# Optimization experiments

Measured on AMD Instinct MI355X. Metric: run time of the kernel, lower is better.

## Reference

```python
import jax, jax.numpy as jnp
import numpy as np

L = 10
DIL = tuple(2 ** i for i in range(L))  # dilations 1..512, kernel_size=2 -> one past tap, mem_size = dilation
DMAX = max(DIL)
R = 64            # residual channels
G = 2 * R         # gate channels (tanh | sigmoid)
S = 256           # skip channels
MEL = 80
NCLS = 256
HOP = 64
END = 256
FRAMES = 8


def setup_inputs() -> dict:
    ks = jax.random.split(jax.random.key(0), 16)
    sc = jnp.float32(0.1)
    n = lambda k, shape: jax.random.normal(k, shape, jnp.float32) * sc
    return {
        "y": jax.random.normal(ks[0], (MEL, FRAMES), jnp.float32),
        "samples": jax.random.uniform(ks[1], (FRAMES * HOP,), jnp.float32),
        "c": 1,
        "emb": jnp.tanh(n(ks[2], (NCLS, R))),               # buffer already tanh'ed in __init__
        "condition_W": n(ks[3], (L * G, MEL)),
        "WV_past_weight": n(ks[4], (L, G, R, 1)),            # kernel_size=2 -> 1 past tap
        "WV_present_weight": n(ks[5], (L, G, R)),
        "W_o_weight": n(ks[6], (L - 1, R + S, R)),
        "W_o_bias": n(ks[7], (L - 1, R + S)),
        "W_o_weight_last": n(ks[8], (S, R)),
        "W_o_bias_last": n(ks[9], (S,)),
        "end1_w": n(ks[10], (END, S)),
        "end1_b": n(ks[11], (END,)),
        "end2_w": n(ks[12], (NCLS, END)),
        "end2_b": n(ks[13], (NCLS,)),
    }


def _forward(y, samples, c, emb, condition_W, WV_past, WV_pres, W_o_w, W_o_b,
             W_o_wl, W_o_bl, e1w, e1b, e2w, e2b):
    # nearest-neighbor upsample of conditioning by hop_length (F.interpolate default mode)
    y_up = jnp.repeat(y, HOP, axis=1)                        # [MEL, T]
    T = y_up.shape[1]
    conds = (condition_W @ y_up).T.reshape(T, L, G)          # precompute all conditioning projections
    dil = jnp.array(DIL, jnp.int32)
    lidx = jnp.arange(L)

    def step(carry, xs):
        hist, prev = carry                                   # hist: [L, R, DMAX] shared ring buffer, global write ptr t%DMAX
        t, cond_t, s = xs
        x = emb[prev]                                        # [R]
        # value written dil[j] steps ago (zeros before warm-up), read before this step's write
        past = hist[lidx, :, (t - dil) % DMAX]               # [L, R]
        skip = jnp.zeros((S,), hist.dtype)
        written = []
        for j in range(L):
            h = cond_t[j] + WV_past[j, :, :, 0] @ past[j] + WV_pres[j] @ x
            zw, zf = jnp.split(h, 2)
            z = jnp.tanh(zw) * jax.nn.sigmoid(zf)
            written.append(x)                                # layer j stores its input in its ring buffer
            if j < L - 1:
                o = W_o_w[j] @ z + W_o_b[j]
                x = x + o[:R]
                skip = skip + o[R:]
            else:
                skip = skip + W_o_wl @ z + W_o_bl
        hist = hist.at[:, :, t % DMAX].set(jnp.stack(written))
        hid = jax.nn.relu(e1w @ jax.nn.relu(skip) + e1b)
        logits = (e2w @ hid + e2b) * c
        # inverse-CDF sampling: first index where cumsum(softmax) exceeds the uniform sample
        new = jnp.argmax(jnp.cumsum(jax.nn.softmax(logits)) > s).astype(jnp.int32)
        return (hist, new), (new, logits)

    carry0 = (jnp.zeros((L, R, DMAX), jnp.float32), jnp.int32(NCLS // 2 - 1))
    _, (outs, logits) = jax.lax.scan(step, carry0, (jnp.arange(T), conds, samples))
    return outs, logits


def reference(y, samples, c, emb, condition_W, WV_past_weight, WV_present_weight,
              W_o_weight, W_o_bias, W_o_weight_last, W_o_bias_last,
              end1_w, end1_b, end2_w, end2_b):
    outs, _ = _forward(y, samples, c, emb, condition_W, WV_past_weight,
                       WV_present_weight, W_o_weight, W_o_bias,
                       W_o_weight_last, W_o_bias_last, end1_w, end1_b, end2_w, end2_b)
    return outs
```

## Files before the change

### kernel.cpp

```cpp
#include <hip/hip_runtime.h>
#include <cmath>

#define L_     10
#define R_     64
#define G_     128
#define S_     256
#define MEL_   80
#define NCLS_  256
#define HOP_   64
#define END_   256
#define FRAMES_ 8
#define T_     512

typedef unsigned long long u64;

#define COND8_OFF   0
#define HIST_OFF    10240
#define MBX64_OFF   (HIST_OFF + 8*T_*R_)
#define CTR64_OFF   (MBX64_OFF + 4*R_*2)
#define HID64_OFF   (CTR64_OFF + 10*S_*2)
#define FLAG_OFF    (HID64_OFF + S_*2)

#define FID_PREV   11
#define FID_CLAIM  12

#define NROLE 7
#define SPIN_CAP (1 << 16)

__device__ __forceinline__ void push_tag(u64* p, float v, int tag) {
  u64 pk = ((u64)(unsigned)tag << 32) | (unsigned)__float_as_int(v);
  asm volatile("global_atomic_swap_x2 %0, %1, off" :: "v"(p), "v"(pk) : "memory");
}
__device__ __forceinline__ float poll_tag(u64* p, int want) {
  u64 r; int n = 0;
  do {
    asm volatile("global_atomic_add_x2 %0, %1, %2, off sc0\n\ts_waitcnt vmcnt(0)"
                 : "=&v"(r) : "v"(p), "v"(0ULL) : "memory");
    if ((int)(r >> 32) >= want) break;
  } while (++n <= SPIN_CAP);
  return __int_as_float((int)(unsigned)(r & 0xffffffffULL));
}
__device__ __forceinline__ float2 poll_tag2(u64* p0, u64* p1, int want) {
  u64 r0, r1; int n = 0;
  for (;;) {
    asm volatile("global_atomic_add_x2 %0, %2, %4, off sc0\n\t"
                 "global_atomic_add_x2 %1, %3, %4, off sc0\n\t"
                 "s_waitcnt vmcnt(0)"
                 : "=&v"(r0), "=&v"(r1) : "v"(p0), "v"(p1), "v"(0ULL) : "memory");
    if ((int)(r0 >> 32) >= want && (int)(r1 >> 32) >= want) break;
    if (++n > SPIN_CAP) break;
  }
  return make_float2(__int_as_float((int)(unsigned)(r0 & 0xffffffffULL)),
                     __int_as_float((int)(unsigned)(r1 & 0xffffffffULL)));
}
__device__ __forceinline__ int flag_poll_atomic(int* p) {
  int v;
  asm volatile("global_atomic_add %0, %1, %2, off sc0\n\ts_waitcnt vmcnt(0)"
               : "=&v"(v) : "v"(p), "v"(0) : "memory");
  return v;
}
__device__ __forceinline__ void push_flag(int* p, int v) {
  asm volatile("global_atomic_swap %0, %1, off" :: "v"(p), "v"(v) : "memory");
}
__device__ __forceinline__ int wait_prev_wave(int* p, int want, int lane) {
  int v = 0, n = 0;
  do {
    if (lane == 0) v = flag_poll_atomic(p);
    v = __shfl(v, 0, 64);
    if ((v >> 16) >= want) break;
  } while (++n <= SPIN_CAP);
  return v & 0xffff;
}

#define DOTREG(N4, W, V4, ACC) do { \
  _Pragma("unroll") \
  for (int k_ = 0; k_ < (N4); ++k_) { float4 a_ = (V4)[k_]; \
    ACC = fmaf((W)[4*k_+0], a_.x, ACC); ACC = fmaf((W)[4*k_+1], a_.y, ACC); \
    ACC = fmaf((W)[4*k_+2], a_.z, ACC); ACC = fmaf((W)[4*k_+3], a_.w, ACC); } \
} while (0)

#define DOTREG_RELU(N4, W, V4, ACC) do { \
  _Pragma("unroll") \
  for (int k_ = 0; k_ < (N4); ++k_) { float4 a_ = (V4)[k_]; \
    a_.x = fmaxf(a_.x, 0.f); a_.y = fmaxf(a_.y, 0.f); \
    a_.z = fmaxf(a_.z, 0.f); a_.w = fmaxf(a_.w, 0.f); \
    ACC = fmaf((W)[4*k_+0], a_.x, ACC); ACC = fmaf((W)[4*k_+1], a_.y, ACC); \
    ACC = fmaf((W)[4*k_+2], a_.z, ACC); ACC = fmaf((W)[4*k_+3], a_.w, ACC); } \
} while (0)

__global__ void cond_prep_kernel(const float* __restrict__ condW,
                                 const float* __restrict__ y,
                                 float* __restrict__ cond8) {
  int idx = blockIdx.x * blockDim.x + threadIdx.x;
  if (idx >= FRAMES_ * L_ * G_) return;
  int f = idx / (L_ * G_);
  int row = idx - f * (L_ * G_);
  float acc = 0.f;
  for (int m = 0; m < MEL_; ++m)
    acc = fmaf(condW[row * MEL_ + m], y[m * FRAMES_ + f], acc);
  cond8[f * (L_ * G_) + row] = acc;
}

__global__ __launch_bounds__(256, 1) void wavenet_pipe(
    const float* __restrict__ samples,
    const int*   __restrict__ c_ptr,
    const float* __restrict__ emb,
    const float* __restrict__ WVp,
    const float* __restrict__ WVx,
    const float* __restrict__ Wo,
    const float* __restrict__ Wob,
    const float* __restrict__ Wol,
    const float* __restrict__ Wobl,
    const float* __restrict__ e1w,
    const float* __restrict__ e1b,
    const float* __restrict__ e2w,
    const float* __restrict__ e2b,
    float* __restrict__ ws,
    int*   __restrict__ out) {

  const int tid = threadIdx.x;

  float* cond8   = ws + COND8_OFF;
  float* hist    = ws + HIST_OFF;
  u64*   mbx     = (u64*)(ws + MBX64_OFF);
  u64*   contrib = (u64*)(ws + CTR64_OFF);
  u64*   mbhid   = (u64*)(ws + HID64_OFF);
  int*   flags   = (int*)(ws + FLAG_OFF);
  int*   fprev   = flags + FID_PREV * 16;

  __shared__ __align__(16) float x_s[R_];
  __shared__ __align__(16) float xb_s[R_];
  __shared__ __align__(16) float z_s[R_];
  __shared__ __align__(16) float zb_s[R_];
  __shared__ __align__(16) float cond_a_s[FRAMES_ * G_];
  __shared__ __align__(16) float cond_b_s[FRAMES_ * G_];
  __shared__ __align__(16) float biasC_s[10 * S_];
  __shared__ __align__(16) float vec_s[S_];
  __shared__ float wred[4], wsum[4];
  __shared__ int wcand[4];
  __shared__ int role_s;

  {
    unsigned xcc;
    asm volatile("s_getreg_b32 %0, hwreg(HW_REG_XCC_ID)" : "=s"(xcc));
    if (tid == 0) {
      int r = -1;
      if (xcc == 0) {
        int c0 = atomicAdd(flags + FID_CLAIM * 16, 1);
        if (c0 < NROLE) r = c0;
      }
      role_s = r;
    }
    __syncthreads();
  }
  const int bid = role_s;
  if (bid < 0) return;

  if (bid < 5) {
    const int k = bid;
    const int j_a = 2 * k, j_b = 2 * k + 1;
    const int dil_a = 1 << j_a, dil_b = 1 << j_b;
    const int gr = tid >> 1, gh = tid & 1;

    float wxa_w[32], wxa_f[32], wxb_w[32], wxb_f[32];
    float woa0[64], wob0[64], wex[64];
    float ba0, bb0;
    if (tid < 128) {
      const float4* p;
      p = (const float4*)(WVx + ((size_t)(j_a * G_ + gr)) * R_ + gh * 32);
      #pragma unroll
      for (int i = 0; i < 8; ++i) ((float4*)wxa_w)[i] = p[i];
      p = (const float4*)(WVx + ((size_t)(j_a * G_ + gr + 64)) * R_ + gh * 32);
      #pragma unroll
      for (int i = 0; i < 8; ++i) ((float4*)wxa_f)[i] = p[i];
      p = (const float4*)(WVx + ((size_t)(j_b * G_ + gr)) * R_ + gh * 32);
      #pragma unroll
      for (int i = 0; i < 8; ++i) ((float4*)wxb_w)[i] = p[i];
      p = (const float4*)(WVx + ((size_t)(j_b * G_ + gr + 64)) * R_ + gh * 32);
      #pragma unroll
      for (int i = 0; i < 8; ++i) ((float4*)wxb_f)[i] = p[i];
    }
    {
      const float* q = Wo + ((size_t)(j_a * (R_ + S_) + tid)) * R_;
      #pragma unroll
      for (int i = 0; i < 64; ++i) woa0[i] = q[i];
      ba0 = Wob[j_a * (R_ + S_) + tid];
      if (k < 4) {
        q = Wo + ((size_t)(j_b * (R_ + S_) + tid)) * R_;
        #pragma unroll
        for (int i = 0; i < 64; ++i) wob0[i] = q[i];
        bb0 = Wob[j_b * (R_ + S_) + tid];
      } else {
        q = Wol + (size_t)tid * R_;
        #pragma unroll
        for (int i = 0; i < 64; ++i) wob0[i] = q[i];
        bb0 = 0.f;
      }
      if (tid < 64) {
        q = Wo + ((size_t)(j_a * (R_ + S_) + 256 + tid)) * R_;
        #pragma unroll
        for (int i = 0; i < 64; ++i) wex[i] = q[i];
      } else if (tid < 128 && k < 4) {
        q = Wo + ((size_t)(j_b * (R_ + S_) + 256 + (tid - 64))) * R_;
        #pragma unroll
        for (int i = 0; i < 64; ++i) wex[i] = q[i];
      }
    }
    for (int i = tid; i < FRAMES_ * G_; i += 256) {
      cond_a_s[i] = cond8[(i >> 7) * (L_ * G_) + j_a * G_ + (i & 127)];
      cond_b_s[i] = cond8[(i >> 7) * (L_ * G_) + j_b * G_ + (i & 127)];
    }
    __syncthreads();
    float pd_aw = 0.f, pd_af = 0.f, pd_bw = 0.f, pd_bf = 0.f;
    if (tid < 128 && gh == 0) {
      pd_aw = cond_a_s[gr]; pd_af = cond_a_s[gr + 64];
      pd_bw = cond_b_s[gr]; pd_bf = cond_b_s[gr + 64];
    }

    float* hist_a = (k > 0) ? (hist + (size_t)(j_a - 1) * T_ * R_) : nullptr;
    float* hist_b = (k < 4) ? (hist + (size_t)(j_b - 1) * T_ * R_) : nullptr;
    u64* mbx_in    = mbx + (size_t)(k - 1) * R_;
    u64* mbx_out   = mbx + (size_t)k * R_;
    u64* contrib_a = contrib + (size_t)j_a * S_;
    u64* contrib_b = contrib + (size_t)j_b * S_;

    for (int t = 0; t < T_; ++t) {
      if (tid < 64) {
        if (k == 0) {
          int prev = 127;
          if (t > 0) prev = wait_prev_wave(fprev, t, tid);
          if (tid < 16)
            ((float4*)x_s)[tid] = ((const float4*)(emb + (size_t)prev * R_))[tid];
        } else {
          x_s[tid] = poll_tag(mbx_in + tid, t + 1);
        }
      }
      __syncthreads();

      if (tid < 128) {
        const float4* xs4 = (const float4*)(x_s + gh * 32);
        float vw = 0.f, vf = 0.f;
        DOTREG(8, wxa_w, xs4, vw);
        DOTREG(8, wxa_f, xs4, vf);
        vw += __shfl_down(vw, 1, 2);
        vf += __shfl_down(vf, 1, 2);
        if (gh == 0) {
          float hw = vw + pd_aw, hf = vf + pd_af;
          z_s[gr] = tanhf(hw) * (1.f / (1.f + expf(-hf)));
        }
      }
      if (hist_a && tid >= 240)
        ((float4*)(hist_a + (size_t)t * R_))[tid - 240] = ((const float4*)x_s)[tid - 240];
      __syncthreads();

      float va_keep = 0.f;
      {
        const float4* z4 = (const float4*)z_s;
        if (tid < 64) {
          float v0 = 0.f, v1 = 0.f;
          DOTREG(16, woa0, z4, v0);
          DOTREG(16, wex, z4, v1);
          xb_s[tid] = x_s[tid] + v0 + ba0;
          va_keep = v1;
        } else {
          float v0 = 0.f;
          DOTREG(16, woa0, z4, v0);
          va_keep = v0;
        }
      }
      __syncthreads();

      if (tid < 128) {
        const float4* xs4 = (const float4*)(xb_s + gh * 32);
        float vw = 0.f, vf = 0.f;
        DOTREG(8, wxb_w, xs4, vw);
        DOTREG(8, wxb_f, xs4, vf);
        vw += __shfl_down(vw, 1, 2);
        vf += __shfl_down(vf, 1, 2);
        if (gh == 0) {
          float hw = vw + pd_bw, hf = vf + pd_bf;
          zb_s[gr] = tanhf(hw) * (1.f / (1.f + expf(-hf)));
        }
      }
      if (hist_b && tid >= 240)
        ((float4*)(hist_b + (size_t)t * R_))[tid - 240] = ((const float4*)xb_s)[tid - 240];
      __syncthreads();

      {
        const float4* zb4 = (const float4*)zb_s;
        float v0 = 0.f;
        DOTREG(16, wob0, zb4, v0);
        if (k < 4) {
          if (tid < 64) {
            push_tag(mbx_out + tid, xb_s[tid] + v0 + bb0, t + 1);
            push_tag(contrib_a + 192 + tid, va_keep, t + 1);
          } else if (tid < 128) {
            float v1 = 0.f;
            DOTREG(16, wex, zb4, v1);
            push_tag(contrib_a + (tid - 64), va_keep, t + 1);
            push_tag(contrib_b + (tid - 64), v0, t + 1);
            push_tag(contrib_b + 192 + (tid - 64), v1, t + 1);
          } else {
            push_tag(contrib_a + (tid - 64), va_keep, t + 1);
            push_tag(contrib_b + (tid - 64), v0, t + 1);
          }
        } else {
          if (tid < 64) {
            push_tag(contrib_b + tid, v0, t + 1);
            push_tag(contrib_a + 192 + tid, va_keep, t + 1);
          } else {
            push_tag(contrib_a + (tid - 64), va_keep, t + 1);
            push_tag(contrib_b + tid, v0, t + 1);
          }
        }
      }

      const int tn = t + 1;
      if (tn < T_ && tid < 128) {
        const int f1 = tn >> 6;
        float wpw[32], wpf[32], pa[32];
        {
          const float4* pw = (const float4*)(WVp + ((size_t)(j_a * G_ + gr)) * R_ + gh * 32);
          const float4* pf = (const float4*)(WVp + ((size_t)(j_a * G_ + gr + 64)) * R_ + gh * 32);
          #pragma unroll
          for (int i = 0; i < 8; ++i) { ((float4*)wpw)[i] = pw[i]; ((float4*)wpf)[i] = pf[i]; }
          if (k == 0) {
            #pragma unroll
            for (int i = 0; i < 8; ++i) ((float4*)pa)[i] = ((const float4*)(x_s + gh * 32))[i];
          } else {
            const int tp = tn - dil_a;
            if (tp >= 0) {
              const float4* hp = (const float4*)(hist_a + (size_t)tp * R_ + gh * 32);
              #pragma unroll
              for (int i = 0; i < 8; ++i) ((float4*)pa)[i] = hp[i];
            } else {
              #pragma unroll
              for (int i = 0; i < 32; ++i) pa[i] = 0.f;
            }
          }
          float vw = 0.f, vf = 0.f;
          const float4* pa4 = (const float4*)pa;
          DOTREG(8, wpw, pa4, vw);
          DOTREG(8, wpf, pa4, vf);
          vw += __shfl_down(vw, 1, 2);
          vf += __shfl_down(vf, 1, 2);
          if (gh == 0) {
            pd_aw = vw + cond_a_s[f1 * G_ + gr];
            pd_af = vf + cond_a_s[f1 * G_ + gr + 64];
          }
        }
        if (k < 4) {
          const float4* pw = (const float4*)(WVp + ((size_t)(j_b * G_ + gr)) * R_ + gh * 32);
          const float4* pf = (const float4*)(WVp + ((size_t)(j_b * G_ + gr + 64)) * R_ + gh * 32);
          #pragma unroll
          for (int i = 0; i < 8; ++i) { ((float4*)wpw)[i] = pw[i]; ((float4*)wpf)[i] = pf[i]; }
          const int tp = tn - dil_b;
          if (tp >= 0) {
            const float4* hp = (const float4*)(hist_b + (size_t)tp * R_ + gh * 32);
            #pragma unroll
            for (int i = 0; i < 8; ++i) ((float4*)pa)[i] = hp[i];
          } else {
            #pragma unroll
            for (int i = 0; i < 32; ++i) pa[i] = 0.f;
          }
          float vw = 0.f, vf = 0.f;
          const float4* pa4 = (const float4*)pa;
          DOTREG(8, wpw, pa4, vw);
          DOTREG(8, wpf, pa4, vf);
          vw += __shfl_down(vw, 1, 2);
          vf += __shfl_down(vf, 1, 2);
          if (gh == 0) {
            pd_bw = vw + cond_b_s[f1 * G_ + gr];
            pd_bf = vf + cond_b_s[f1 * G_ + gr + 64];
          }
        } else {
          if (gh == 0) {
            pd_bw = cond_b_s[f1 * G_ + gr];
            pd_bf = cond_b_s[f1 * G_ + gr + 64];
          }
        }
      }
      __syncthreads();
    }

  } else if (bid == 5) {
    const int o_loc = tid >> 1, halfc = tid & 1;
    float w0[128], w1[128];
    {
      const float* p = e1w + ((size_t)o_loc) * S_ + halfc * 128;
      #pragma unroll
      for (int i = 0; i < 128; ++i) w0[i] = p[i];
      p = e1w + ((size_t)(128 + o_loc)) * S_ + halfc * 128;
      #pragma unroll
      for (int i = 0; i < 128; ++i) w1[i] = p[i];
    }
    const float bias0 = e1b[o_loc], bias1 = e1b[128 + o_loc];
    for (int i = tid; i < 10 * S_; i += 256) {
      int j = i >> 8, s = i & 255;
      biasC_s[i] = (j < 9) ? Wob[j * (R_ + S_) + 64 + s] : Wobl[s];
    }
    __syncthreads();

    for (int t = 0; t < T_; ++t) {
      float sacc = 0.f;
      for (int kk = 0; kk < 5; ++kk) {
        float2 v = poll_tag2(contrib + (size_t)(2 * kk) * S_ + tid,
                             contrib + (size_t)(2 * kk + 1) * S_ + tid, t + 1);
        sacc = (sacc + v.x) + biasC_s[(2 * kk) * S_ + tid];
        sacc = (sacc + v.y) + biasC_s[(2 * kk + 1) * S_ + tid];
      }
      vec_s[tid] = sacc;
      __syncthreads();
      const float4* s4 = (const float4*)(vec_s + halfc * 128);
      float v0 = 0.f, v1 = 0.f;
      DOTREG_RELU(32, w0, s4, v0);
      v0 += __shfl_down(v0, 1, 2);
      DOTREG_RELU(32, w1, s4, v1);
      v1 += __shfl_down(v1, 1, 2);
      if (halfc == 0) {
        push_tag(mbhid + o_loc,       fmaxf(v0 + bias0, 0.f), t + 1);
        push_tag(mbhid + 128 + o_loc, fmaxf(v1 + bias1, 0.f), t + 1);
      }
      __syncthreads();
    }

  } else {
    const int o_loc = tid >> 1, halfc = tid & 1;
    const float cf = (float)c_ptr[0];
    float w0[128], w1[128];
    {
      const float* p = e2w + ((size_t)o_loc) * END_ + halfc * 128;
      #pragma unroll
      for (int i = 0; i < 128; ++i) w0[i] = p[i];
      p = e2w + ((size_t)(128 + o_loc)) * END_ + halfc * 128;
      #pragma unroll
      for (int i = 0; i < 128; ++i) w1[i] = p[i];
    }
    const float bias0 = e2b[o_loc], bias1 = e2b[128 + o_loc];
    float* logits_s = cond_b_s;
    const int lane = tid & 63, wv = tid >> 6;

    for (int t = 0; t < T_; ++t) {
      vec_s[tid] = poll_tag(mbhid + tid, t + 1);
      __syncthreads();
      const float4* h4 = (const float4*)(vec_s + halfc * 128);
      float v0 = 0.f, v1 = 0.f;
      DOTREG(32, w0, h4, v0);
      v0 += __shfl_down(v0, 1, 2);
      DOTREG(32, w1, h4, v1);
      v1 += __shfl_down(v1, 1, 2);
      if (halfc == 0) {
        logits_s[o_loc]       = (v0 + bias0) * cf;
        logits_s[128 + o_loc] = (v1 + bias1) * cf;
      }
      __syncthreads();

      float lg = logits_s[tid];
      float m = lg;
      #pragma unroll
      for (int off = 32; off >= 1; off >>= 1) m = fmaxf(m, __shfl_xor(m, off, 64));
      if (lane == 0) wred[wv] = m;
      __syncthreads();
      m = fmaxf(fmaxf(wred[0], wred[1]), fmaxf(wred[2], wred[3]));
      float e = expf(lg - m);
      float cs = e;
      #pragma unroll
      for (int off = 1; off < 64; off <<= 1) {
        float o_ = __shfl_up(cs, off, 64);
        if (lane >= off) cs += o_;
      }
      if (lane == 63) wsum[wv] = cs;
      __syncthreads();
      float total = wsum[0] + wsum[1] + wsum[2] + wsum[3];
      float offv = 0.f;
      for (int w2 = 0; w2 < wv; ++w2) offv += wsum[w2];
      float thresh = samples[t] * total;
      bool flagb = (offv + cs) > thresh;
      unsigned long long mk = __ballot(flagb);
      if (lane == 0) wcand[wv] = mk ? (wv * 64 + __ffsll(mk) - 1) : 100000;
      __syncthreads();
      if (tid == 0) {
        int nw = min(min(wcand[0], wcand[1]), min(wcand[2], wcand[3]));
        if (nw >= 100000) nw = 0;
        out[t] = nw;
        push_flag(fprev, ((t + 1) << 16) | nw);
      }
      __syncthreads();
    }
  }
}

extern "C" void kernel_launch(void* const* d_in, const int* in_sizes, int n_in,
                              void* d_out, int out_size, void* d_ws, size_t ws_size,
                              hipStream_t stream) {
  const float* y       = (const float*)d_in[0];
  const float* samples = (const float*)d_in[1];
  const int*   c       = (const int*)d_in[2];
  const float* emb     = (const float*)d_in[3];
  const float* condW   = (const float*)d_in[4];
  const float* WVp     = (const float*)d_in[5];
  const float* WVx     = (const float*)d_in[6];
  const float* Wo      = (const float*)d_in[7];
  const float* Wob     = (const float*)d_in[8];
  const float* Wol     = (const float*)d_in[9];
  const float* Wobl    = (const float*)d_in[10];
  const float* e1w     = (const float*)d_in[11];
  const float* e1b     = (const float*)d_in[12];
  const float* e2w     = (const float*)d_in[13];
  const float* e2b     = (const float*)d_in[14];

  float* ws  = (float*)d_ws;
  int*   out = (int*)d_out;

  hipMemsetAsync((char*)d_ws + (size_t)FLAG_OFF * sizeof(float), 0,
                 16 * 16 * sizeof(int), stream);

  cond_prep_kernel<<<(FRAMES_ * L_ * G_ + 255) / 256, 256, 0, stream>>>(
      condW, y, ws + COND8_OFF);

  wavenet_pipe<<<256, 256, 0, stream>>>(samples, c, emb, WVp, WVx, Wo, Wob,
                                        Wol, Wobl, e1w, e1b, e2w, e2b, ws, out);
}
```

Baseline: 8.852 ms.

## Split layer blocks into critical-path wave and helper waves synced via LDS counters

Within each two-layer block, one 64-thread wave now runs the serial residual chain (gate dots, residual projections, mailbox push) with full 64-wide weight rows in registers. The other three waves compute the skip contributions, the history writes and the next step's past-tap projections. The two groups coordinate through LDS atomic counters instead of block-wide __syncthreads, so only the critical chain sits on the inter-block latency path. The cost is the spin-wait overhead on the counters and heavier register use per lane, since each thread now computes a full 64-length dot product with no lane-pair split.

```diff
diff --git a/kernel.cpp b/kernel.cpp
--- a/kernel.cpp
+++ b/kernel.cpp
@@ -26,6 +26,7 @@
 
 #define NROLE 7
 #define SPIN_CAP (1 << 16)
+#define LDS_SPIN_CAP (1 << 17)
 
 __device__ __forceinline__ void push_tag(u64* p, float v, int tag) {
   u64 pk = ((u64)(unsigned)tag << 32) | (unsigned)__float_as_int(v);
@@ -70,6 +71,19 @@
     if ((v >> 16) >= want) break;
   } while (++n <= SPIN_CAP);
   return v & 0xffff;
+}
+
+__device__ __forceinline__ void lds_spin_ge(int* p, int want) {
+  int n = 0;
+  while (__hip_atomic_load(p, __ATOMIC_ACQUIRE, __HIP_MEMORY_SCOPE_WORKGROUP) < want) {
+    if (++n > LDS_SPIN_CAP) break;
+  }
+}
+__device__ __forceinline__ void lds_store_rel(int* p, int v) {
+  __hip_atomic_store(p, v, __ATOMIC_RELEASE, __HIP_MEMORY_SCOPE_WORKGROUP);
+}
+__device__ __forceinline__ void lds_add_rel(int* p) {
+  (void)__hip_atomic_fetch_add(p, 1, __ATOMIC_RELEASE, __HIP_MEMORY_SCOPE_WORKGROUP);
 }
 
 #define DOTREG(N4, W, V4, ACC) do { \
@@ -130,8 +144,10 @@
 
   __shared__ __align__(16) float x_s[R_];
   __shared__ __align__(16) float xb_s[R_];
-  __shared__ __align__(16) float z_s[R_];
-  __shared__ __align__(16) float zb_s[R_];
+  __shared__ __align__(16) float z_sa[R_];
+  __shared__ __align__(16) float z_sb[R_];
+  __shared__ __align__(16) float pd_sa[G_];
+  __shared__ __align__(16) float pd_sb[G_];
   __shared__ __align__(16) float cond_a_s[FRAMES_ * G_];
   __shared__ __align__(16) float cond_b_s[FRAMES_ * G_];
   __shared__ __align__(16) float biasC_s[10 * S_];
@@ -139,6 +155,7 @@
   __shared__ float wred[4], wsum[4];
   __shared__ int wcand[4];
   __shared__ int role_s;
+  __shared__ int zctr, cdone;
 
   {
     unsigned xcc;
@@ -150,6 +167,7 @@
         if (c0 < NROLE) r = c0;
       }
       role_s = r;
+      zctr = 0; cdone = 0;
     }
     __syncthreads();
   }
@@ -160,62 +178,6 @@
     const int k = bid;
     const int j_a = 2 * k, j_b = 2 * k + 1;
     const int dil_a = 1 << j_a, dil_b = 1 << j_b;
-    const int gr = tid >> 1, gh = tid & 1;
-
-    float wxa_w[32], wxa_f[32], wxb_w[32], wxb_f[32];
-    float woa0[64], wob0[64], wex[64];
-    float ba0, bb0;
-    if (tid < 128) {
-      const float4* p;
-      p = (const float4*)(WVx + ((size_t)(j_a * G_ + gr)) * R_ + gh * 32);
-      #pragma unroll
-      for (int i = 0; i < 8; ++i) ((float4*)wxa_w)[i] = p[i];
-      p = (const float4*)(WVx + ((size_t)(j_a * G_ + gr + 64)) * R_ + gh * 32);
-      #pragma unroll
-      for (int i = 0; i < 8; ++i) ((float4*)wxa_f)[i] = p[i];
-      p = (const float4*)(WVx + ((size_t)(j_b * G_ + gr)) * R_ + gh * 32);
-      #pragma unroll
-      for (int i = 0; i < 8; ++i) ((float4*)wxb_w)[i] = p[i];
-      p = (const float4*)(WVx + ((size_t)(j_b * G_ + gr + 64)) * R_ + gh * 32);
-      #pragma unroll
-      for (int i = 0; i < 8; ++i) ((float4*)wxb_f)[i] = p[i];
-    }
-    {
-      const float* q = Wo + ((size_t)(j_a * (R_ + S_) + tid)) * R_;
-      #pragma unroll
-      for (int i = 0; i < 64; ++i) woa0[i] = q[i];
-      ba0 = Wob[j_a * (R_ + S_) + tid];
-      if (k < 4) {
-        q = Wo + ((size_t)(j_b * (R_ + S_) + tid)) * R_;
-        #pragma unroll
-        for (int i = 0; i < 64; ++i) wob0[i] = q[i];
-        bb0 = Wob[j_b * (R_ + S_) + tid];
-      } else {
-        q = Wol + (size_t)tid * R_;
-        #pragma unroll
-        for (int i = 0; i < 64; ++i) wob0[i] = q[i];
-        bb0 = 0.f;
-      }
-      if (tid < 64) {
-        q = Wo + ((size_t)(j_a * (R_ + S_) + 256 + tid)) * R_;
-        #pragma unroll
-        for (int i = 0; i < 64; ++i) wex[i] = q[i];
-      } else if (tid < 128 && k < 4) {
-        q = Wo + ((size_t)(j_b * (R_ + S_) + 256 + (tid - 64))) * R_;
-        #pragma unroll
-        for (int i = 0; i < 64; ++i) wex[i] = q[i];
-      }
-    }
-    for (int i = tid; i < FRAMES_ * G_; i += 256) {
-      cond_a_s[i] = cond8[(i >> 7) * (L_ * G_) + j_a * G_ + (i & 127)];
-      cond_b_s[i] = cond8[(i >> 7) * (L_ * G_) + j_b * G_ + (i & 127)];
-    }
-    __syncthreads();
-    float pd_aw = 0.f, pd_af = 0.f, pd_bw = 0.f, pd_bf = 0.f;
-    if (tid < 128 && gh == 0) {
-      pd_aw = cond_a_s[gr]; pd_af = cond_a_s[gr + 64];
-      pd_bw = cond_b_s[gr]; pd_bf = cond_b_s[gr + 64];
-    }
 
     float* hist_a = (k > 0) ? (hist + (size_t)(j_a - 1) * T_ * R_) : nullptr;
     float* hist_b = (k < 4) ? (hist + (size_t)(j_b - 1) * T_ * R_) : nullptr;
@@ -224,163 +186,200 @@
     u64* contrib_a = contrib + (size_t)j_a * S_;
     u64* contrib_b = contrib + (size_t)j_b * S_;
 
-    for (int t = 0; t < T_; ++t) {
-      if (tid < 64) {
+    for (int i = tid; i < FRAMES_ * G_; i += 256) {
+      cond_a_s[i] = cond8[(i >> 7) * (L_ * G_) + j_a * G_ + (i & 127)];
+      cond_b_s[i] = cond8[(i >> 7) * (L_ * G_) + j_b * G_ + (i & 127)];
+    }
+
+    if (tid < 64) {
+      const int r = tid;
+      float gw_a[64], gf_a[64], gw_b[64], gf_b[64], wres_a[64], wres_b[64];
+      float ba0 = 0.f, bb0 = 0.f;
+      {
+        const float4* p;
+        p = (const float4*)(WVx + ((size_t)(j_a * G_ + r)) * R_);
+        #pragma unroll
+        for (int i = 0; i < 16; ++i) ((float4*)gw_a)[i] = p[i];
+        p = (const float4*)(WVx + ((size_t)(j_a * G_ + r + 64)) * R_);
+        #pragma unroll
+        for (int i = 0; i < 16; ++i) ((float4*)gf_a)[i] = p[i];
+        p = (const float4*)(WVx + ((size_t)(j_b * G_ + r)) * R_);
+        #pragma unroll
+        for (int i = 0; i < 16; ++i) ((float4*)gw_b)[i] = p[i];
+        p = (const float4*)(WVx + ((size_t)(j_b * G_ + r + 64)) * R_);
+        #pragma unroll
+        for (int i = 0; i < 16; ++i) ((float4*)gf_b)[i] = p[i];
+        p = (const float4*)(Wo + ((size_t)(j_a * (R_ + S_) + r)) * R_);
+        #pragma unroll
+        for (int i = 0; i < 16; ++i) ((float4*)wres_a)[i] = p[i];
+        ba0 = Wob[j_a * (R_ + S_) + r];
+        if (k < 4) {
+          p = (const float4*)(Wo + ((size_t)(j_b * (R_ + S_) + r)) * R_);
+          #pragma unroll
+          for (int i = 0; i < 16; ++i) ((float4*)wres_b)[i] = p[i];
+          bb0 = Wob[j_b * (R_ + S_) + r];
+        } else {
+          p = (const float4*)(Wol + (size_t)r * R_);
+          #pragma unroll
+          for (int i = 0; i < 16; ++i) ((float4*)wres_b)[i] = p[i];
+        }
+      }
+      __syncthreads();
+
+      for (int t = 0; t < T_; ++t) {
+        lds_spin_ge(&cdone, 3 * t);
+
+        float x;
         if (k == 0) {
           int prev = 127;
-          if (t > 0) prev = wait_prev_wave(fprev, t, tid);
-          if (tid < 16)
-            ((float4*)x_s)[tid] = ((const float4*)(emb + (size_t)prev * R_))[tid];
+          if (t > 0) prev = wait_prev_wave(fprev, t, r);
+          x = emb[(size_t)prev * R_ + r];
         } else {
-          x_s[tid] = poll_tag(mbx_in + tid, t + 1);
-        }
-      }
-      __syncthreads();
-
-      if (tid < 128) {
-        const float4* xs4 = (const float4*)(x_s + gh * 32);
-        float vw = 0.f, vf = 0.f;
-        DOTREG(8, wxa_w, xs4, vw);
-        DOTREG(8, wxa_f, xs4, vf);
-        vw += __shfl_down(vw, 1, 2);
-        vf += __shfl_down(vf, 1, 2);
-        if (gh == 0) {
-          float hw = vw + pd_aw, hf = vf + pd_af;
-          z_s[gr] = tanhf(hw) * (1.f / (1.f + expf(-hf)));
-        }
-      }
-      if (hist_a && tid >= 240)
-        ((float4*)(hist_a + (size_t)t * R_))[tid - 240] = ((const float4*)x_s)[tid - 240];
-      __syncthreads();
-
-      float va_keep = 0.f;
+          x = poll_tag(mbx_in + r, t + 1);
+        }
+        x_s[r] = x;
+
+        {
+          const float4* x4 = (const float4*)x_s;
+          float pdw = pd_sa[r], pdf = pd_sa[64 + r];
+          float a0 = 0.f, a1 = 0.f, b0 = 0.f, b1 = 0.f;
+          DOTREG(8, gw_a, x4, a0);       DOTREG(8, gw_a + 32, x4 + 8, a1);
+          DOTREG(8, gf_a, x4, b0);       DOTREG(8, gf_a + 32, x4 + 8, b1);
+          float hw = (a0 + a1) + pdw, hf = (b0 + b1) + pdf;
+          z_sa[r] = tanhf(hw) * (1.f / (1.f + expf(-hf)));
+        }
+        if (r == 0) lds_store_rel(&zctr, 2 * t + 1);
+
+        float xb;
+        {
+          float v0 = 0.f;
+          DOTREG(16, wres_a, (const float4*)z_sa, v0);
+          xb = x + v0 + ba0;
+          xb_s[r] = xb;
+        }
+
+        {
+          const float4* x4 = (const float4*)xb_s;
+          float pdw = pd_sb[r], pdf = pd_sb[64 + r];
+          float a0 = 0.f, a1 = 0.f, b0 = 0.f, b1 = 0.f;
+          DOTREG(8, gw_b, x4, a0);       DOTREG(8, gw_b + 32, x4 + 8, a1);
+          DOTREG(8, gf_b, x4, b0);       DOTREG(8, gf_b + 32, x4 + 8, b1);
+          float hw = (a0 + a1) + pdw, hf = (b0 + b1) + pdf;
+          z_sb[r] = tanhf(hw) * (1.f / (1.f + expf(-hf)));
+        }
+        if (r == 0) lds_store_rel(&zctr, 2 * t + 2);
+
+        {
+          float v0 = 0.f;
+          DOTREG(16, wres_b, (const float4*)z_sb, v0);
+          if (k < 4) push_tag(mbx_out + r, xb + v0 + bb0, t + 1);
+          else       push_tag(contrib_b + r, v0, t + 1);
+        }
+      }
+
+    } else {
+      const int u = tid - 64;
+      float wca1[64], wca2[64], wcb1[64], wcb2[64];
       {
-        const float4* z4 = (const float4*)z_s;
-        if (tid < 64) {
-          float v0 = 0.f, v1 = 0.f;
-          DOTREG(16, woa0, z4, v0);
-          DOTREG(16, wex, z4, v1);
-          xb_s[tid] = x_s[tid] + v0 + ba0;
-          va_keep = v1;
-        } else {
-          float v0 = 0.f;
-          DOTREG(16, woa0, z4, v0);
-          va_keep = v0;
-        }
-      }
-      __syncthreads();
-
-      if (tid < 128) {
-        const float4* xs4 = (const float4*)(xb_s + gh * 32);
-        float vw = 0.f, vf = 0.f;
-        DOTREG(8, wxb_w, xs4, vw);
-        DOTREG(8, wxb_f, xs4, vf);
-        vw += __shfl_down(vw, 1, 2);
-        vf += __shfl_down(vf, 1, 2);
-        if (gh == 0) {
-          float hw = vw + pd_bw, hf = vf + pd_bf;
-          zb_s[gr] = tanhf(hw) * (1.f / (1.f + expf(-hf)));
-        }
-      }
-      if (hist_b && tid >= 240)
-        ((float4*)(hist_b + (size_t)t * R_))[tid - 240] = ((const float4*)xb_s)[tid - 240];
-      __syncthreads();
-
-      {
-        const float4* zb4 = (const float4*)zb_s;
-        float v0 = 0.f;
-        DOTREG(16, wob0, zb4, v0);
+        const float4* p;
+        p = (const float4*)(Wo + ((size_t)(j_a * (R_ + S_) + 64 + u)) * R_);
+        #pragma unroll
+        for (int i = 0; i < 16; ++i) ((float4*)wca1)[i] = p[i];
+        if (u < 64) {
+          p = (const float4*)(Wo + ((size_t)(j_a * (R_ + S_) + 256 + u)) * R_);
+          #pragma unroll
+          for (int i = 0; i < 16; ++i) ((float4*)wca2)[i] = p[i];
+        }
         if (k < 4) {
-          if (tid < 64) {
-            push_tag(mbx_out + tid, xb_s[tid] + v0 + bb0, t + 1);
-            push_tag(contrib_a + 192 + tid, va_keep, t + 1);
-          } else if (tid < 128) {
-            float v1 = 0.f;
-            DOTREG(16, wex, zb4, v1);
-            push_tag(contrib_a + (tid - 64), va_keep, t + 1);
-            push_tag(contrib_b + (tid - 64), v0, t + 1);
-            push_tag(contrib_b + 192 + (tid - 64), v1, t + 1);
-          } else {
-            push_tag(contrib_a + (tid - 64), va_keep, t + 1);
-            push_tag(contrib_b + (tid - 64), v0, t + 1);
+          p = (const float4*)(Wo + ((size_t)(j_b * (R_ + S_) + 64 + u)) * R_);
+          #pragma unroll
+          for (int i = 0; i < 16; ++i) ((float4*)wcb1)[i] = p[i];
+          if (u < 64) {
+            p = (const float4*)(Wo + ((size_t)(j_b * (R_ + S_) + 256 + u)) * R_);
+            #pragma unroll
+            for (int i = 0; i < 16; ++i) ((float4*)wcb2)[i] = p[i];
           }
         } else {
-          if (tid < 64) {
-            push_tag(contrib_b + tid, v0, t + 1);
-            push_tag(contrib_a + 192 + tid, va_keep, t + 1);
+          p = (const float4*)(Wol + (size_t)(64 + u) * R_);
+          #pragma unroll
+          for (int i = 0; i < 16; ++i) ((float4*)wcb1)[i] = p[i];
+        }
+      }
+      if (u >= 64) {
+        const int pr = u - 64;
+        pd_sa[pr] = cond_a_s[pr];
+        pd_sb[pr] = cond_b_s[pr];
+      }
+      __syncthreads();
+
+      for (int t = 0; t < T_; ++t) {
+        lds_spin_ge(&zctr, 2 * t + 1);
+        {
+          float v = 0.f;
+          DOTREG(16, wca1, (const float4*)z_sa, v);
+          push_tag(contrib_a + u, v, t + 1);
+          if (u < 64) {
+            float v2 = 0.f;
+            DOTREG(16, wca2, (const float4*)z_sa, v2);
+            push_tag(contrib_a + 192 + u, v2, t + 1);
+          }
+        }
+        if (k > 0 && u >= 176)
+          ((float4*)(hist_a + (size_t)t * R_))[u - 176] = ((const float4*)x_s)[u - 176];
+
+        lds_spin_ge(&zctr, 2 * t + 2);
+        {
+          float v = 0.f;
+          DOTREG(16, wcb1, (const float4*)z_sb, v);
+          push_tag(contrib_b + ((k < 4) ? u : (64 + u)), v, t + 1);
+          if (k < 4 && u < 64) {
+            float v2 = 0.f;
+            DOTREG(16, wcb2, (const float4*)z_sb, v2);
+            push_tag(contrib_b + 192 + u, v2, t + 1);
+          }
+        }
+        if (k < 4 && u >= 160 && u < 176)
+          ((float4*)(hist_b + (size_t)t * R_))[u - 160] = ((const float4*)xb_s)[u - 160];
+
+        const int tn = t + 1;
+        if (tn < T_ && u >= 64) {
+          const int pr = u - 64;
+          const int f1 = tn >> 6;
+          float wtmp[64];
+          {
+            const float4* wp4 = (const float4*)(WVp + ((size_t)(j_a * G_ + pr)) * R_);
+            #pragma unroll
+            for (int i = 0; i < 16; ++i) ((float4*)wtmp)[i] = wp4[i];
+            float a0 = 0.f, a1 = 0.f;
+            if (k == 0) {
+              const float4* p4 = (const float4*)x_s;
+              DOTREG(8, wtmp, p4, a0);  DOTREG(8, wtmp + 32, p4 + 8, a1);
+            } else {
+              const int tp = tn - dil_a;
+              if (tp >= 0) {
+                const float4* p4 = (const float4*)(hist_a + (size_t)tp * R_);
+                DOTREG(8, wtmp, p4, a0);  DOTREG(8, wtmp + 32, p4 + 8, a1);
+              }
+            }
+            pd_sa[pr] = (a0 + a1) + cond_a_s[f1 * G_ + pr];
+          }
+          if (k < 4) {
+            const float4* wp4 = (const float4*)(WVp + ((size_t)(j_b * G_ + pr)) * R_);
+            #pragma unroll
+            for (int i = 0; i < 16; ++i) ((float4*)wtmp)[i] = wp4[i];
+            float a0 = 0.f, a1 = 0.f;
+            const int tp = tn - dil_b;
+            if (tp >= 0) {
+              const float4* p4 = (const float4*)(hist_b + (size_t)tp * R_);
+              DOTREG(8, wtmp, p4, a0);  DOTREG(8, wtmp + 32, p4 + 8, a1);
+            }
+            pd_sb[pr] = (a0 + a1) + cond_b_s[f1 * G_ + pr];
           } else {
-            push_tag(contrib_a + (tid - 64), va_keep, t + 1);
-            push_tag(contrib_b + tid, v0, t + 1);
+            pd_sb[pr] = cond_b_s[f1 * G_ + pr];
           }
         }
-      }
-
-      const int tn = t + 1;
-      if (tn < T_ && tid < 128) {
-        const int f1 = tn >> 6;
-        float wpw[32], wpf[32], pa[32];
-        {
-          const float4* pw = (const float4*)(WVp + ((size_t)(j_a * G_ + gr)) * R_ + gh * 32);
-          const float4* pf = (const float4*)(WVp + ((size_t)(j_a * G_ + gr + 64)) * R_ + gh * 32);
-          #pragma unroll
-          for (int i = 0; i < 8; ++i) { ((float4*)wpw)[i] = pw[i]; ((float4*)wpf)[i] = pf[i]; }
-          if (k == 0) {
-            #pragma unroll
-            for (int i = 0; i < 8; ++i) ((float4*)pa)[i] = ((const float4*)(x_s + gh * 32))[i];
-          } else {
-            const int tp = tn - dil_a;
-            if (tp >= 0) {
-              const float4* hp = (const float4*)(hist_a + (size_t)tp * R_ + gh * 32);
-              #pragma unroll
-              for (int i = 0; i < 8; ++i) ((float4*)pa)[i] = hp[i];
-            } else {
-              #pragma unroll
-              for (int i = 0; i < 32; ++i) pa[i] = 0.f;
-            }
-          }
-          float vw = 0.f, vf = 0.f;
-          const float4* pa4 = (const float4*)pa;
-          DOTREG(8, wpw, pa4, vw);
-          DOTREG(8, wpf, pa4, vf);
-          vw += __shfl_down(vw, 1, 2);
-          vf += __shfl_down(vf, 1, 2);
-          if (gh == 0) {
-            pd_aw = vw + cond_a_s[f1 * G_ + gr];
-            pd_af = vf + cond_a_s[f1 * G_ + gr + 64];
-          }
-        }
-        if (k < 4) {
-          const float4* pw = (const float4*)(WVp + ((size_t)(j_b * G_ + gr)) * R_ + gh * 32);
-          const float4* pf = (const float4*)(WVp + ((size_t)(j_b * G_ + gr + 64)) * R_ + gh * 32);
-          #pragma unroll
-          for (int i = 0; i < 8; ++i) { ((float4*)wpw)[i] = pw[i]; ((float4*)wpf)[i] = pf[i]; }
-          const int tp = tn - dil_b;
-          if (tp >= 0) {
-            const float4* hp = (const float4*)(hist_b + (size_t)tp * R_ + gh * 32);
-            #pragma unroll
-            for (int i = 0; i < 8; ++i) ((float4*)pa)[i] = hp[i];
-          } else {
-            #pragma unroll
-            for (int i = 0; i < 32; ++i) pa[i] = 0.f;
-          }
-          float vw = 0.f, vf = 0.f;
-          const float4* pa4 = (const float4*)pa;
-          DOTREG(8, wpw, pa4, vw);
-          DOTREG(8, wpf, pa4, vf);
-          vw += __shfl_down(vw, 1, 2);
-          vf += __shfl_down(vf, 1, 2);
-          if (gh == 0) {
-            pd_bw = vw + cond_b_s[f1 * G_ + gr];
-            pd_bf = vf + cond_b_s[f1 * G_ + gr + 64];
-          }
-        } else {
-          if (gh == 0) {
-            pd_bw = cond_b_s[f1 * G_ + gr];
-            pd_bf = cond_b_s[f1 * G_ + gr + 64];
-          }
-        }
-      }
-      __syncthreads();
+        if ((u & 63) == 0) lds_add_rel(&cdone);
+      }
     }
 
   } else if (bid == 5) {
```

Measured after the change: 10.31 ms. +16.4%, slower.
